# Kernel optimization log

Hardware: AMD Instinct MI355X
Metric: run time of the kernel (lower is better)

Reference implementation:

```python
import jax, jax.numpy as jnp
import numpy as np

B, H, N, D = 2, 16, 2048, 128

def setup_inputs() -> dict:
    key = jax.random.key(0)
    kq, kk, kv = jax.random.split(key, 3)
    q = jax.random.normal(kq, (B, H, N, D), dtype=jnp.float32)
    k = jax.random.normal(kk, (B, H, N, D), dtype=jnp.float32)
    v = jax.random.normal(kv, (B, H, N, D), dtype=jnp.float32)
    return {"q": q, "k": k, "v": v}

def reference(q, k, v):
    # scale = 1/sqrt(d) computed at forward time (scale=None in __init__)
    d = q.shape[-1]
    scale = 1.0 / jnp.sqrt(jnp.asarray(d, dtype=q.dtype))
    # scores: (B, H, N, N)
    scores = jnp.einsum('bhnd,bhmd->bhnm', q, k) * scale
    probs = jax.nn.softmax(scores, axis=-1)
    return jnp.einsum('bhnm,bhmd->bhnd', probs, v)
```

## Files before the change

### kernel.cpp

```cpp
#include <hip/hip_runtime.h>
#include <hip/hip_bf16.h>
#include <stdint.h>

#define BATCH 2
#define HEADS 16
#define BH    32
#define SEQ   2048
#define DIM   128
#define ELEMS (BATCH*HEADS*SEQ*DIM)

#define KVB   64
#define NT    (SEQ/KVB)

using f32x4  = __attribute__((ext_vector_type(4))) float;
using f32x16 = __attribute__((ext_vector_type(16))) float;
using bf16x8 = __attribute__((ext_vector_type(8))) short;
using us4    = __attribute__((ext_vector_type(4))) unsigned short;

__device__ __forceinline__ unsigned short f2bf(float f) {
    union { float f; uint32_t u; } v; v.f = f;
    uint32_t u = v.u;
    uint32_t r = u + 0x7FFFu + ((u >> 16) & 1u);
    return (unsigned short)(r >> 16);
}

__device__ __forceinline__ uint32_t packbf2(float lo, float hi) {
    __hip_bfloat162 h2 = __float22bfloat162_rn(make_float2(lo, hi));
    union { __hip_bfloat162 h; uint32_t u; } c; c.h = h2;
    return c.u;
}

__global__ __launch_bounds__(256) void prep(const float* __restrict__ Q,
                                            const float* __restrict__ K,
                                            const float* __restrict__ V,
                                            unsigned short* __restrict__ qb,
                                            unsigned short* __restrict__ kb,
                                            unsigned short* __restrict__ vt) {
    const int b = blockIdx.x, t = threadIdx.x;
    const float scl = 0.08838834764831845f * 1.4426950408889634f;
    if (b < 4096) {
        const bool isQ = b < 2048;
        const float* src = isQ ? Q : K;
        unsigned short* dst = isQ ? qb : kb;
        const float f = isQ ? scl : 1.0f;
        size_t base = (size_t)(isQ ? b : b - 2048) * 4096 + t * 4;
        #pragma unroll
        for (int j = 0; j < 4; ++j) {
            f32x4 v = *(const f32x4*)(src + base + j * 1024);
            us4 o;
            #pragma unroll
            for (int jj = 0; jj < 4; ++jj) o[jj] = f2bf(v[jj] * f);
            *(us4*)(dst + base + j * 1024) = o;
        }
    } else {
        __shared__ unsigned short tile[64][66];
        const int b2 = b - 4096;
        const int bh = b2 >> 6, rem = b2 & 63;
        const int n0 = (rem >> 1) * 64, d0 = (rem & 1) * 64;
        const int rr = t >> 4, cc = t & 15;
        #pragma unroll
        for (int j = 0; j < 4; ++j) {
            int row = rr + 16 * j;
            f32x4 v = *(const f32x4*)(V + ((size_t)bh * SEQ + n0 + row) * DIM + d0 + cc * 4);
            #pragma unroll
            for (int jj = 0; jj < 4; ++jj) tile[row][cc * 4 + jj] = f2bf(v[jj]);
        }
        __syncthreads();
        #pragma unroll
        for (int j = 0; j < 4; ++j) {
            int drow = rr + 16 * j;
            us4 o;
            #pragma unroll
            for (int jj = 0; jj < 4; ++jj) o[jj] = tile[cc * 4 + jj][drow];
            *(us4*)(vt + ((size_t)bh * DIM + d0 + drow) * SEQ + n0 + cc * 4) = o;
        }
    }
}

__global__ __launch_bounds__(256, 2) void attn_fwd(const unsigned short* __restrict__ Qb,
                                                   const unsigned short* __restrict__ Kb,
                                                   const unsigned short* __restrict__ VTb,
                                                   float* __restrict__ Out) {
    __shared__ __attribute__((aligned(16))) char smem[65536];

    const int bid  = blockIdx.x;
    const int xcd  = bid & 7;
    const int slot = bid >> 3;
    const int head = xcd * 4 + (slot >> 4);
    const int wid  = threadIdx.x >> 6;
    const int lane = threadIdx.x & 63;
    const int l31  = lane & 31;
    const int hL   = lane >> 5;
    const int q0   = (slot & 15) * 128 + wid * 32;

    const unsigned short* Qh = Qb + (size_t)head * SEQ * DIM;
    const char* KhB  = (const char*)(Kb  + (size_t)head * SEQ * DIM);
    const char* VThB = (const char*)(VTb + (size_t)head * DIM * SEQ);

    bf16x8 qf[8];
    {
        const char* qrow = (const char*)(Qh + (size_t)(q0 + l31) * DIM) + 16 * hL;
        #pragma unroll
        for (int u = 0; u < 8; ++u) qf[u] = *(const bf16x8*)(qrow + 32 * u);
    }

    f32x16 acc[4];
    #pragma unroll
    for (int m = 0; m < 4; ++m) acc[m] = (f32x16)(0.f);
    float m_run = -INFINITY, l_run = 0.f;

    const int swzK = (l31 & 15) << 4;
    const int swzV = ((l31 >> 1) & 7) << 4;

    auto STAGE = [&](int buf, int kv0) {
        #pragma unroll
        for (int i = 0; i < 4; ++i) {
            int seg = wid * 4 + i;
            int r   = seg * 4 + (lane >> 4);
            int cb  = ((lane & 15) << 4) ^ ((r & 15) << 4);
            const char* g = KhB + (((size_t)(kv0 + r)) << 8) + cb;
            __builtin_amdgcn_global_load_lds(
                (const __attribute__((address_space(1))) void*)g,
                (__attribute__((address_space(3))) void*)(smem + buf * 16384 + seg * 1024),
                16, 0, 0);
        }
        #pragma unroll
        for (int i = 0; i < 4; ++i) {
            int seg = wid * 4 + i;
            int rp  = seg * 4 + (lane >> 4);
            int q8  = (lane & 15) << 4;
            int pre = q8 ^ ((rp & 7) << 4);
            int r   = 2 * rp + (pre >> 7);
            int cb  = pre & 127;
            const char* g = VThB + (size_t)r * (SEQ * 2) + ((size_t)kv0 << 1) + cb;
            __builtin_amdgcn_global_load_lds(
                (const __attribute__((address_space(1))) void*)g,
                (__attribute__((address_space(3))) void*)(smem + 32768 + buf * 16384 + seg * 1024),
                16, 0, 0);
        }
    };

    STAGE(0, 0);

    for (int t = 0; t < NT; ++t) {
        const int cur = t & 1;
        if (t + 1 < NT) {
            STAGE(cur ^ 1, (t + 1) * KVB);
            asm volatile("s_waitcnt vmcnt(8)" ::: "memory");
        } else {
            asm volatile("s_waitcnt vmcnt(0)" ::: "memory");
        }
        __builtin_amdgcn_s_barrier();
        asm volatile("" ::: "memory");

        const char* kb = smem + cur * 16384;
        const char* vb = smem + 32768 + cur * 16384;

        f32x16 s0 = (f32x16)(0.f), s1 = (f32x16)(0.f);
        {
            const char* krow0 = kb + (size_t)l31 * 256;
            const char* krow1 = kb + (size_t)(32 + l31) * 256;
            #pragma unroll
            for (int u = 0; u < 8; ++u) {
                int cb = (32 * u + 16 * hL) ^ swzK;
                bf16x8 k0 = *(const bf16x8*)(krow0 + cb);
                bf16x8 k1 = *(const bf16x8*)(krow1 + cb);
                s0 = __builtin_amdgcn_mfma_f32_32x32x16_bf16(k0, qf[u], s0, 0, 0, 0);
                s1 = __builtin_amdgcn_mfma_f32_32x32x16_bf16(k1, qf[u], s1, 0, 0, 0);
            }
        }

        float smax = -1e30f;
        #pragma unroll
        for (int r = 0; r < 16; ++r)
            smax = fmaxf(smax, fmaxf(s0[r], s1[r]));
        smax = fmaxf(smax, __shfl_xor(smax, 32));

        if (!__all(smax - m_run <= 8.f)) {
            float mnew = fmaxf(m_run, smax);
            float corr = __builtin_amdgcn_exp2f(m_run - mnew);
            #pragma unroll
            for (int m = 0; m < 4; ++m) acc[m] *= corr;
            l_run *= corr;
            m_run = mnew;
        }

        float psum = 0.f;
        #pragma unroll
        for (int r = 0; r < 16; ++r) {
            s0[r] = __builtin_amdgcn_exp2f(s0[r] - m_run);
            s1[r] = __builtin_amdgcn_exp2f(s1[r] - m_run);
            psum += s0[r] + s1[r];
        }
        l_run += psum;

        uint32_t w0[8], w1[8];
        #pragma unroll
        for (int k2 = 0; k2 < 8; ++k2) {
            w0[k2] = packbf2(s0[2 * k2], s0[2 * k2 + 1]);
            w1[k2] = packbf2(s1[2 * k2], s1[2 * k2 + 1]);
        }

        #pragma unroll
        for (int tt = 0; tt < 2; ++tt) {
            #pragma unroll
            for (int ssi = 0; ssi < 2; ++ssi) {
                uint32_t A0 = tt ? w1[4 * ssi]     : w0[4 * ssi];
                uint32_t A1 = tt ? w1[4 * ssi + 1] : w0[4 * ssi + 1];
                uint32_t C0 = tt ? w1[4 * ssi + 2] : w0[4 * ssi + 2];
                uint32_t C1 = tt ? w1[4 * ssi + 3] : w0[4 * ssi + 3];
                uint32_t o0 = hL ? A0 : C0;
                uint32_t o1 = hL ? A1 : C1;
                uint32_t e0 = (uint32_t)__shfl_xor((int)o0, 32);
                uint32_t e1 = (uint32_t)__shfl_xor((int)o1, 32);
                union { uint32_t u[4]; bf16x8 v; } Bf;
                Bf.u[0] = hL ? e0 : A0;
                Bf.u[1] = hL ? e1 : A1;
                Bf.u[2] = hL ? C0 : e0;
                Bf.u[3] = hL ? C1 : e1;
                const int cbv = (32 * (2 * tt + ssi) + 16 * hL) + ((l31 & 1) << 7);
                #pragma unroll
                for (int m = 0; m < 4; ++m) {
                    int rp = 16 * m + (l31 >> 1);
                    bf16x8 vf = *(const bf16x8*)(vb + (size_t)rp * 256 + (cbv ^ swzV));
                    acc[m] = __builtin_amdgcn_mfma_f32_32x32x16_bf16(vf, Bf.v, acc[m], 0, 0, 0);
                }
            }
        }

        asm volatile("" ::: "memory");
        __builtin_amdgcn_s_barrier();
    }

    __syncthreads();
    const float l_tot = l_run + __shfl_xor(l_run, 32);
    const float inv = 1.0f / l_tot;
    float* ob = (float*)(smem + wid * 16384);
    #pragma unroll
    for (int m = 0; m < 4; ++m) {
        #pragma unroll
        for (int r = 0; r < 16; ++r) {
            int d = 32 * m + (r & 3) + 8 * (r >> 2) + 4 * hL;
            ob[l31 * 128 + (d ^ ((l31 & 7) << 2))] = acc[m][r] * inv;
        }
    }
    __syncthreads();
    {
        float* outp = Out + ((size_t)head * SEQ + q0) * DIM;
        #pragma unroll
        for (int i = 0; i < 16; ++i) {
            int row = 2 * i + hL;
            f32x4 v = *(const f32x4*)(ob + row * 128 + ((4 * l31) ^ ((row & 7) << 2)));
            *(f32x4*)(outp + (size_t)row * DIM + 4 * l31) = v;
        }
    }
}

extern "C" void kernel_launch(void* const* d_in, const int* in_sizes, int n_in,
                              void* d_out, int out_size, void* d_ws, size_t ws_size,
                              hipStream_t stream) {
    (void)in_sizes; (void)n_in; (void)out_size;
    const float* q = (const float*)d_in[0];
    const float* k = (const float*)d_in[1];
    const float* v = (const float*)d_in[2];
    float* out = (float*)d_out;

    const size_t needed = (size_t)ELEMS * 2 * 3;
    if (ws_size < needed) return;

    unsigned short* qb = (unsigned short*)d_ws;
    unsigned short* kb = qb + ELEMS;
    unsigned short* vt = kb + ELEMS;

    prep<<<6144, 256, 0, stream>>>(q, k, v, qb, kb, vt);
    attn_fwd<<<512, 256, 0, stream>>>(qb, kb, vt, out);
}
```

Measured before the change: 219.2 us.

## Software-pipeline QK^T of next tile with softmax/PV of current tile

```diff
diff --git a/kernel.cpp b/kernel.cpp
--- a/kernel.cpp
+++ b/kernel.cpp
@@ -112,7 +112,7 @@
     const int swzK = (l31 & 15) << 4;
     const int swzV = ((l31 >> 1) & 7) << 4;
 
-    auto STAGE = [&](int buf, int kv0) {
+    auto STAGE_K = [&](int buf, int kv0) {
         #pragma unroll
         for (int i = 0; i < 4; ++i) {
             int seg = wid * 4 + i;
@@ -124,6 +124,8 @@
                 (__attribute__((address_space(3))) void*)(smem + buf * 16384 + seg * 1024),
                 16, 0, 0);
         }
+    };
+    auto STAGE_V = [&](int buf, int kv0) {
         #pragma unroll
         for (int i = 0; i < 4; ++i) {
             int seg = wid * 4 + i;
@@ -140,97 +142,122 @@
         }
     };
 
-    STAGE(0, 0);
-
-    for (int t = 0; t < NT; ++t) {
-        const int cur = t & 1;
-        if (t + 1 < NT) {
-            STAGE(cur ^ 1, (t + 1) * KVB);
-            asm volatile("s_waitcnt vmcnt(8)" ::: "memory");
-        } else {
-            asm volatile("s_waitcnt vmcnt(0)" ::: "memory");
-        }
-        __builtin_amdgcn_s_barrier();
-        asm volatile("" ::: "memory");
-
-        const char* kb = smem + cur * 16384;
-        const char* vb = smem + 32768 + cur * 16384;
-
-        f32x16 s0 = (f32x16)(0.f), s1 = (f32x16)(0.f);
-        {
-            const char* krow0 = kb + (size_t)l31 * 256;
-            const char* krow1 = kb + (size_t)(32 + l31) * 256;
-            #pragma unroll
-            for (int u = 0; u < 8; ++u) {
-                int cb = (32 * u + 16 * hL) ^ swzK;
-                bf16x8 k0 = *(const bf16x8*)(krow0 + cb);
-                bf16x8 k1 = *(const bf16x8*)(krow1 + cb);
-                s0 = __builtin_amdgcn_mfma_f32_32x32x16_bf16(k0, qf[u], s0, 0, 0, 0);
-                s1 = __builtin_amdgcn_mfma_f32_32x32x16_bf16(k1, qf[u], s1, 0, 0, 0);
-            }
-        }
-
-        float smax = -1e30f;
-        #pragma unroll
-        for (int r = 0; r < 16; ++r)
-            smax = fmaxf(smax, fmaxf(s0[r], s1[r]));
-        smax = fmaxf(smax, __shfl_xor(smax, 32));
-
-        if (!__all(smax - m_run <= 8.f)) {
-            float mnew = fmaxf(m_run, smax);
-            float corr = __builtin_amdgcn_exp2f(m_run - mnew);
-            #pragma unroll
-            for (int m = 0; m < 4; ++m) acc[m] *= corr;
-            l_run *= corr;
-            m_run = mnew;
-        }
-
-        float psum = 0.f;
-        #pragma unroll
-        for (int r = 0; r < 16; ++r) {
-            s0[r] = __builtin_amdgcn_exp2f(s0[r] - m_run);
-            s1[r] = __builtin_amdgcn_exp2f(s1[r] - m_run);
-            psum += s0[r] + s1[r];
-        }
-        l_run += psum;
-
-        uint32_t w0[8], w1[8];
-        #pragma unroll
-        for (int k2 = 0; k2 < 8; ++k2) {
-            w0[k2] = packbf2(s0[2 * k2], s0[2 * k2 + 1]);
-            w1[k2] = packbf2(s1[2 * k2], s1[2 * k2 + 1]);
-        }
-
-        #pragma unroll
-        for (int tt = 0; tt < 2; ++tt) {
-            #pragma unroll
-            for (int ssi = 0; ssi < 2; ++ssi) {
-                uint32_t A0 = tt ? w1[4 * ssi]     : w0[4 * ssi];
-                uint32_t A1 = tt ? w1[4 * ssi + 1] : w0[4 * ssi + 1];
-                uint32_t C0 = tt ? w1[4 * ssi + 2] : w0[4 * ssi + 2];
-                uint32_t C1 = tt ? w1[4 * ssi + 3] : w0[4 * ssi + 3];
-                uint32_t o0 = hL ? A0 : C0;
-                uint32_t o1 = hL ? A1 : C1;
-                uint32_t e0 = (uint32_t)__shfl_xor((int)o0, 32);
-                uint32_t e1 = (uint32_t)__shfl_xor((int)o1, 32);
-                union { uint32_t u[4]; bf16x8 v; } Bf;
-                Bf.u[0] = hL ? e0 : A0;
-                Bf.u[1] = hL ? e1 : A1;
-                Bf.u[2] = hL ? C0 : e0;
-                Bf.u[3] = hL ? C1 : e1;
-                const int cbv = (32 * (2 * tt + ssi) + 16 * hL) + ((l31 & 1) << 7);
-                #pragma unroll
-                for (int m = 0; m < 4; ++m) {
-                    int rp = 16 * m + (l31 >> 1);
-                    bf16x8 vf = *(const bf16x8*)(vb + (size_t)rp * 256 + (cbv ^ swzV));
-                    acc[m] = __builtin_amdgcn_mfma_f32_32x32x16_bf16(vf, Bf.v, acc[m], 0, 0, 0);
-                }
-            }
-        }
-
-        asm volatile("" ::: "memory");
-        __builtin_amdgcn_s_barrier();
-    }
+#define PHASE(SC0, SC1, SN0, SN1, KBUF, VBUF, DO_NEXT, DO_STG, SBUF, STILE) do {     \
+    if (DO_NEXT) { asm volatile("s_waitcnt vmcnt(4)" ::: "memory"); }                \
+    else         { asm volatile("s_waitcnt vmcnt(0)" ::: "memory"); }                \
+    __builtin_amdgcn_s_barrier();                                                    \
+    asm volatile("" ::: "memory");                                                   \
+    if (DO_STG) STAGE_K(SBUF, (STILE) * KVB);                                        \
+    if (DO_NEXT) {                                                                   \
+        SN0 = (f32x16)(0.f); SN1 = (f32x16)(0.f);                                    \
+        const char* krow0_ = (KBUF) + (size_t)l31 * 256;                             \
+        const char* krow1_ = (KBUF) + (size_t)(32 + l31) * 256;                      \
+        _Pragma("unroll")                                                            \
+        for (int u = 0; u < 8; ++u) {                                                \
+            int cb_ = (32 * u + 16 * hL) ^ swzK;                                     \
+            bf16x8 k0_ = *(const bf16x8*)(krow0_ + cb_);                             \
+            bf16x8 k1_ = *(const bf16x8*)(krow1_ + cb_);                             \
+            SN0 = __builtin_amdgcn_mfma_f32_32x32x16_bf16(k0_, qf[u], SN0, 0, 0, 0); \
+            SN1 = __builtin_amdgcn_mfma_f32_32x32x16_bf16(k1_, qf[u], SN1, 0, 0, 0); \
+        }                                                                            \
+    }                                                                                \
+    {                                                                                \
+        float smax_ = -1e30f;                                                        \
+        _Pragma("unroll")                                                            \
+        for (int r = 0; r < 16; ++r)                                                 \
+            smax_ = fmaxf(smax_, fmaxf(SC0[r], SC1[r]));                             \
+        smax_ = fmaxf(smax_, __shfl_xor(smax_, 32));                                 \
+        if (!__all(smax_ - m_run <= 8.f)) {                                          \
+            float mnew_ = fmaxf(m_run, smax_);                                       \
+            float corr_ = __builtin_amdgcn_exp2f(m_run - mnew_);                     \
+            _Pragma("unroll")                                                        \
+            for (int m = 0; m < 4; ++m) acc[m] *= corr_;                             \
+            l_run *= corr_;                                                          \
+            m_run = mnew_;                                                           \
+        }                                                                            \
+        float psum_ = 0.f;                                                           \
+        _Pragma("unroll")                                                            \
+        for (int r = 0; r < 16; ++r) {                                               \
+            SC0[r] = __builtin_amdgcn_exp2f(SC0[r] - m_run);                         \
+            SC1[r] = __builtin_amdgcn_exp2f(SC1[r] - m_run);                         \
+            psum_ += SC0[r] + SC1[r];                                                \
+        }                                                                            \
+        l_run += psum_;                                                              \
+        uint32_t w0_[8], w1_[8];                                                     \
+        _Pragma("unroll")                                                            \
+        for (int k2 = 0; k2 < 8; ++k2) {                                             \
+            w0_[k2] = packbf2(SC0[2 * k2], SC0[2 * k2 + 1]);                         \
+            w1_[k2] = packbf2(SC1[2 * k2], SC1[2 * k2 + 1]);                         \
+        }                                                                            \
+        _Pragma("unroll")                                                            \
+        for (int tj = 0; tj < 2; ++tj) {                                             \
+            _Pragma("unroll")                                                        \
+            for (int ssi = 0; ssi < 2; ++ssi) {                                      \
+                uint32_t A0 = tj ? w1_[4 * ssi]     : w0_[4 * ssi];                  \
+                uint32_t A1 = tj ? w1_[4 * ssi + 1] : w0_[4 * ssi + 1];              \
+                uint32_t C0 = tj ? w1_[4 * ssi + 2] : w0_[4 * ssi + 2];              \
+                uint32_t C1 = tj ? w1_[4 * ssi + 3] : w0_[4 * ssi + 3];              \
+                uint32_t o0 = hL ? A0 : C0;                                          \
+                uint32_t o1 = hL ? A1 : C1;                                          \
+                uint32_t e0 = (uint32_t)__shfl_xor((int)o0, 32);                     \
+                uint32_t e1 = (uint32_t)__shfl_xor((int)o1, 32);                     \
+                union { uint32_t u[4]; bf16x8 v; } Bf;                               \
+                Bf.u[0] = hL ? e0 : A0;                                              \
+                Bf.u[1] = hL ? e1 : A1;                                              \
+                Bf.u[2] = hL ? C0 : e0;                                              \
+                Bf.u[3] = hL ? C1 : e1;                                              \
+                const int cbv_ = (32 * (2 * tj + ssi) + 16 * hL) + ((l31 & 1) << 7); \
+                _Pragma("unroll")                                                    \
+                for (int m = 0; m < 4; ++m) {                                        \
+                    int rp_ = 16 * m + (l31 >> 1);                                   \
+                    bf16x8 vf_ = *(const bf16x8*)((VBUF) + (size_t)rp_ * 256 + (cbv_ ^ swzV)); \
+                    acc[m] = __builtin_amdgcn_mfma_f32_32x32x16_bf16(vf_, Bf.v, acc[m], 0, 0, 0); \
+                }                                                                    \
+            }                                                                        \
+        }                                                                            \
+    }                                                                                \
+    asm volatile("" ::: "memory");                                                   \
+    __builtin_amdgcn_s_barrier();                                                    \
+    if (DO_STG) STAGE_V(SBUF, (STILE) * KVB);                                        \
+} while (0)
+
+    const char* kb0 = smem;
+    const char* kb1 = smem + 16384;
+    const char* vb0 = smem + 32768;
+    const char* vb1 = smem + 32768 + 16384;
+
+    STAGE_K(0, 0);
+    STAGE_K(1, KVB);
+    STAGE_V(0, 0);
+    STAGE_V(1, KVB);
+    asm volatile("s_waitcnt vmcnt(0)" ::: "memory");
+    __builtin_amdgcn_s_barrier();
+    asm volatile("" ::: "memory");
+
+    f32x16 sa0 = (f32x16)(0.f), sa1 = (f32x16)(0.f);
+    f32x16 sb0, sb1;
+    {
+        const char* krow0 = kb0 + (size_t)l31 * 256;
+        const char* krow1 = kb0 + (size_t)(32 + l31) * 256;
+        #pragma unroll
+        for (int u = 0; u < 8; ++u) {
+            int cb = (32 * u + 16 * hL) ^ swzK;
+            bf16x8 k0 = *(const bf16x8*)(krow0 + cb);
+            bf16x8 k1 = *(const bf16x8*)(krow1 + cb);
+            sa0 = __builtin_amdgcn_mfma_f32_32x32x16_bf16(k0, qf[u], sa0, 0, 0, 0);
+            sa1 = __builtin_amdgcn_mfma_f32_32x32x16_bf16(k1, qf[u], sa1, 0, 0, 0);
+        }
+    }
+
+    #pragma unroll 1
+    for (int tt = 0; tt < NT - 2; tt += 2) {
+        PHASE(sa0, sa1, sb0, sb1, kb1, vb0, 1, 1, 0, tt + 2);
+        PHASE(sb0, sb1, sa0, sa1, kb0, vb1, 1, 1, 1, tt + 3);
+    }
+    PHASE(sa0, sa1, sb0, sb1, kb1, vb0, 1, 0, 0, 0);
+    PHASE(sb0, sb1, sa0, sa1, kb0, vb1, 0, 0, 0, 0);
+
+#undef PHASE
 
     __syncthreads();
     const float l_tot = l_run + __shfl_xor(l_run, 32);
```

Measured after the change: 218.7 us. No clear change (-0.2%).

## Halve KV tile to 32 rows, raise occupancy to 3 blocks, use permlane32_swap

Applied to the files above, without the earlier changes.

```diff
diff --git a/kernel.cpp b/kernel.cpp
--- a/kernel.cpp
+++ b/kernel.cpp
@@ -9,13 +9,14 @@
 #define DIM   128
 #define ELEMS (BATCH*HEADS*SEQ*DIM)
 
-#define KVB   64
+#define KVB   32
 #define NT    (SEQ/KVB)
 
 using f32x4  = __attribute__((ext_vector_type(4))) float;
 using f32x16 = __attribute__((ext_vector_type(16))) float;
 using bf16x8 = __attribute__((ext_vector_type(8))) short;
 using us4    = __attribute__((ext_vector_type(4))) unsigned short;
+using ui2    = __attribute__((ext_vector_type(2))) unsigned int;
 
 __device__ __forceinline__ unsigned short f2bf(float f) {
     union { float f; uint32_t u; } v; v.f = f;
@@ -77,11 +78,11 @@
     }
 }
 
-__global__ __launch_bounds__(256, 2) void attn_fwd(const unsigned short* __restrict__ Qb,
+__global__ __launch_bounds__(256, 3) void attn_fwd(const unsigned short* __restrict__ Qb,
                                                    const unsigned short* __restrict__ Kb,
                                                    const unsigned short* __restrict__ VTb,
                                                    float* __restrict__ Out) {
-    __shared__ __attribute__((aligned(16))) char smem[65536];
+    __shared__ __attribute__((aligned(16))) char smem[32768];
 
     const int bid  = blockIdx.x;
     const int xcd  = bid & 7;
@@ -110,70 +111,66 @@
     float m_run = -INFINITY, l_run = 0.f;
 
     const int swzK = (l31 & 15) << 4;
-    const int swzV = ((l31 >> 1) & 7) << 4;
 
     auto STAGE = [&](int buf, int kv0) {
         #pragma unroll
-        for (int i = 0; i < 4; ++i) {
-            int seg = wid * 4 + i;
+        for (int i = 0; i < 2; ++i) {
+            int seg = wid * 2 + i;
             int r   = seg * 4 + (lane >> 4);
             int cb  = ((lane & 15) << 4) ^ ((r & 15) << 4);
             const char* g = KhB + (((size_t)(kv0 + r)) << 8) + cb;
             __builtin_amdgcn_global_load_lds(
                 (const __attribute__((address_space(1))) void*)g,
-                (__attribute__((address_space(3))) void*)(smem + buf * 16384 + seg * 1024),
+                (__attribute__((address_space(3))) void*)(smem + buf * 8192 + seg * 1024),
                 16, 0, 0);
         }
         #pragma unroll
-        for (int i = 0; i < 4; ++i) {
-            int seg = wid * 4 + i;
-            int rp  = seg * 4 + (lane >> 4);
-            int q8  = (lane & 15) << 4;
-            int pre = q8 ^ ((rp & 7) << 4);
-            int r   = 2 * rp + (pre >> 7);
-            int cb  = pre & 127;
+        for (int i = 0; i < 2; ++i) {
+            int seg = wid * 2 + i;
+            int rp  = seg * 8 + (lane >> 3);
+            int c   = (lane & 7) << 4;
+            int pre = c ^ ((rp & 7) << 4);
+            int r   = 2 * rp + ((pre >> 6) & 1);
+            int cb  = pre & 63;
             const char* g = VThB + (size_t)r * (SEQ * 2) + ((size_t)kv0 << 1) + cb;
             __builtin_amdgcn_global_load_lds(
                 (const __attribute__((address_space(1))) void*)g,
-                (__attribute__((address_space(3))) void*)(smem + 32768 + buf * 16384 + seg * 1024),
+                (__attribute__((address_space(3))) void*)(smem + 16384 + buf * 8192 + seg * 1024),
                 16, 0, 0);
         }
     };
 
     STAGE(0, 0);
 
+    #pragma unroll 1
     for (int t = 0; t < NT; ++t) {
         const int cur = t & 1;
         if (t + 1 < NT) {
             STAGE(cur ^ 1, (t + 1) * KVB);
-            asm volatile("s_waitcnt vmcnt(8)" ::: "memory");
+            asm volatile("s_waitcnt vmcnt(4)" ::: "memory");
         } else {
             asm volatile("s_waitcnt vmcnt(0)" ::: "memory");
         }
         __builtin_amdgcn_s_barrier();
         asm volatile("" ::: "memory");
 
-        const char* kb = smem + cur * 16384;
-        const char* vb = smem + 32768 + cur * 16384;
-
-        f32x16 s0 = (f32x16)(0.f), s1 = (f32x16)(0.f);
+        const char* kb = smem + cur * 8192;
+        const char* vb = smem + 16384 + cur * 8192;
+
+        f32x16 s0 = (f32x16)(0.f);
         {
-            const char* krow0 = kb + (size_t)l31 * 256;
-            const char* krow1 = kb + (size_t)(32 + l31) * 256;
+            const char* krow = kb + (size_t)l31 * 256;
             #pragma unroll
             for (int u = 0; u < 8; ++u) {
                 int cb = (32 * u + 16 * hL) ^ swzK;
-                bf16x8 k0 = *(const bf16x8*)(krow0 + cb);
-                bf16x8 k1 = *(const bf16x8*)(krow1 + cb);
+                bf16x8 k0 = *(const bf16x8*)(krow + cb);
                 s0 = __builtin_amdgcn_mfma_f32_32x32x16_bf16(k0, qf[u], s0, 0, 0, 0);
-                s1 = __builtin_amdgcn_mfma_f32_32x32x16_bf16(k1, qf[u], s1, 0, 0, 0);
             }
         }
 
         float smax = -1e30f;
         #pragma unroll
-        for (int r = 0; r < 16; ++r)
-            smax = fmaxf(smax, fmaxf(s0[r], s1[r]));
+        for (int r = 0; r < 16; ++r) smax = fmaxf(smax, s0[r]);
         smax = fmaxf(smax, __shfl_xor(smax, 32));
 
         if (!__all(smax - m_run <= 8.f)) {
@@ -185,46 +182,34 @@
             m_run = mnew;
         }
 
-        float psum = 0.f;
+        float ps[4] = {0.f, 0.f, 0.f, 0.f};
         #pragma unroll
         for (int r = 0; r < 16; ++r) {
             s0[r] = __builtin_amdgcn_exp2f(s0[r] - m_run);
-            s1[r] = __builtin_amdgcn_exp2f(s1[r] - m_run);
-            psum += s0[r] + s1[r];
-        }
-        l_run += psum;
-
-        uint32_t w0[8], w1[8];
-        #pragma unroll
-        for (int k2 = 0; k2 < 8; ++k2) {
+            ps[r & 3] += s0[r];
+        }
+        l_run += (ps[0] + ps[1]) + (ps[2] + ps[3]);
+
+        uint32_t w0[8];
+        #pragma unroll
+        for (int k2 = 0; k2 < 8; ++k2)
             w0[k2] = packbf2(s0[2 * k2], s0[2 * k2 + 1]);
-            w1[k2] = packbf2(s1[2 * k2], s1[2 * k2 + 1]);
-        }
-
-        #pragma unroll
-        for (int tt = 0; tt < 2; ++tt) {
-            #pragma unroll
-            for (int ssi = 0; ssi < 2; ++ssi) {
-                uint32_t A0 = tt ? w1[4 * ssi]     : w0[4 * ssi];
-                uint32_t A1 = tt ? w1[4 * ssi + 1] : w0[4 * ssi + 1];
-                uint32_t C0 = tt ? w1[4 * ssi + 2] : w0[4 * ssi + 2];
-                uint32_t C1 = tt ? w1[4 * ssi + 3] : w0[4 * ssi + 3];
-                uint32_t o0 = hL ? A0 : C0;
-                uint32_t o1 = hL ? A1 : C1;
-                uint32_t e0 = (uint32_t)__shfl_xor((int)o0, 32);
-                uint32_t e1 = (uint32_t)__shfl_xor((int)o1, 32);
-                union { uint32_t u[4]; bf16x8 v; } Bf;
-                Bf.u[0] = hL ? e0 : A0;
-                Bf.u[1] = hL ? e1 : A1;
-                Bf.u[2] = hL ? C0 : e0;
-                Bf.u[3] = hL ? C1 : e1;
-                const int cbv = (32 * (2 * tt + ssi) + 16 * hL) + ((l31 & 1) << 7);
-                #pragma unroll
-                for (int m = 0; m < 4; ++m) {
-                    int rp = 16 * m + (l31 >> 1);
-                    bf16x8 vf = *(const bf16x8*)(vb + (size_t)rp * 256 + (cbv ^ swzV));
-                    acc[m] = __builtin_amdgcn_mfma_f32_32x32x16_bf16(vf, Bf.v, acc[m], 0, 0, 0);
-                }
+
+        #pragma unroll
+        for (int ss = 0; ss < 2; ++ss) {
+            ui2 r02 = __builtin_amdgcn_permlane32_swap(w0[4 * ss],     w0[4 * ss + 2], false, false);
+            ui2 r13 = __builtin_amdgcn_permlane32_swap(w0[4 * ss + 1], w0[4 * ss + 3], false, false);
+            union { uint32_t u[4]; bf16x8 v; } Bf;
+            Bf.u[0] = r02[0];
+            Bf.u[1] = r13[0];
+            Bf.u[2] = r02[1];
+            Bf.u[3] = r13[1];
+            #pragma unroll
+            for (int m = 0; m < 4; ++m) {
+                int rp = 16 * m + (l31 >> 1);
+                int byte = ((((l31 & 1) << 6) | (32 * ss + 16 * hL)) ^ ((rp & 7) << 4));
+                bf16x8 vf = *(const bf16x8*)(vb + (size_t)rp * 128 + byte);
+                acc[m] = __builtin_amdgcn_mfma_f32_32x32x16_bf16(vf, Bf.v, acc[m], 0, 0, 0);
             }
         }
 
@@ -235,24 +220,30 @@
     __syncthreads();
     const float l_tot = l_run + __shfl_xor(l_run, 32);
     const float inv = 1.0f / l_tot;
-    float* ob = (float*)(smem + wid * 16384);
+    float* ob = (float*)(smem + wid * 8192);
     #pragma unroll
-    for (int m = 0; m < 4; ++m) {
-        #pragma unroll
-        for (int r = 0; r < 16; ++r) {
-            int d = 32 * m + (r & 3) + 8 * (r >> 2) + 4 * hL;
-            ob[l31 * 128 + (d ^ ((l31 & 7) << 2))] = acc[m][r] * inv;
-        }
-    }
-    __syncthreads();
-    {
-        float* outp = Out + ((size_t)head * SEQ + q0) * DIM;
-        #pragma unroll
-        for (int i = 0; i < 16; ++i) {
-            int row = 2 * i + hL;
-            f32x4 v = *(const f32x4*)(ob + row * 128 + ((4 * l31) ^ ((row & 7) << 2)));
-            *(f32x4*)(outp + (size_t)row * DIM + 4 * l31) = v;
-        }
+    for (int h = 0; h < 2; ++h) {
+        #pragma unroll
+        for (int mm = 0; mm < 2; ++mm) {
+            int m = 2 * h + mm;
+            #pragma unroll
+            for (int r = 0; r < 16; ++r) {
+                int dl = 32 * mm + (r & 3) + 8 * (r >> 2) + 4 * hL;
+                ob[l31 * 64 + (dl ^ ((l31 & 7) << 2))] = acc[m][r] * inv;
+            }
+        }
+        __syncthreads();
+        {
+            int row = lane >> 1, ch = (lane & 1) * 32;
+            float* dst = Out + ((size_t)head * SEQ + q0 + row) * DIM + 64 * h + ch;
+            const float* src = ob + row * 64;
+            #pragma unroll
+            for (int j = 0; j < 8; ++j) {
+                int col = ch + 4 * j;
+                *(f32x4*)(dst + 4 * j) = *(const f32x4*)(src + (col ^ ((row & 7) << 2)));
+            }
+        }
+        if (h == 0) __syncthreads();
     }
 }
 
```

Result: no change. 217.8 us (-0.6%).
